# Kernel optimization log

Hardware: AMD Instinct MI355X
Metric: run time of the kernel (lower is better)

The kernel has to match this reference:

```python
import jax, jax.numpy as jnp
import numpy as np

D_MODEL = 1024
LN_EPS = 1e-5


def setup_inputs() -> dict:
    key = jax.random.key(0)
    ks = jax.random.split(key, 12)
    d = D_MODEL
    std_qkv = np.sqrt(2.0 / (d + d / 16)).astype(np.float32)
    std_fc = np.sqrt(2.0 / (d + d)).astype(np.float32)  # xavier_normal for square matrix
    inp = {
        "x": jax.random.normal(ks[0], (2, 2048, d), dtype=jnp.float32),
        "Wq": jax.random.normal(ks[1], (d, d), dtype=jnp.float32) * std_qkv,
        "bq": jnp.zeros((d,), dtype=jnp.float32),
        "Wk": jax.random.normal(ks[2], (d, d), dtype=jnp.float32) * std_qkv,
        "bk": jnp.zeros((d,), dtype=jnp.float32),
        "Wv": jax.random.normal(ks[3], (d, d), dtype=jnp.float32) * std_qkv,
        "bv": jnp.zeros((d,), dtype=jnp.float32),
        "Wfc": jax.random.normal(ks[4], (d, d), dtype=jnp.float32) * std_fc,
        "bfc": jnp.zeros((d,), dtype=jnp.float32),
        "gamma": jnp.ones((d,), dtype=jnp.float32),
        "beta": jnp.zeros((d,), dtype=jnp.float32),
        "n_heads": 16,
    }
    return inp


def reference(x, Wq, bq, Wk, bk, Wv, bv, Wfc, bfc, gamma, beta, n_heads):
    b, l, d = x.shape
    dk = d // n_heads

    def proj2(t, W, bias):
        # Faithful to original: projection applied TWICE (w_qs(w_qs(input)) etc.)
        t = t @ W.T + bias
        return t @ W.T + bias

    def split_heads(t):
        # b l (h dk) -> h b l dk
        return t.reshape(b, l, n_heads, dk).transpose(2, 0, 1, 3)

    q = split_heads(proj2(x, Wq, bq))
    k = split_heads(proj2(x, Wk, bk))
    v = split_heads(proj2(x, Wv, bv))

    scores = jnp.einsum("hblk,hbtk->hblt", q, k) / np.sqrt(dk).astype(np.float32)
    attn = jax.nn.softmax(scores, axis=3)
    out = jnp.einsum("hblt,hbtv->hblv", attn, v)
    out = out.transpose(1, 2, 0, 3).reshape(b, l, d)  # h b l v -> b l (h v)
    out = out @ Wfc.T + bfc  # dropout = identity in eval
    out = out + x

    mu = jnp.mean(out, axis=-1, keepdims=True)
    var = jnp.mean(jnp.square(out - mu), axis=-1, keepdims=True)
    out = (out - mu) * jax.lax.rsqrt(var + LN_EPS) * gamma + beta
    return (out, attn)
```

## Files before the change

kernel.cpp:

```cpp
#include <hip/hip_runtime.h>
#include <hip/hip_bf16.h>

typedef unsigned short u16;
typedef float  f32x4  __attribute__((ext_vector_type(4)));
typedef short  bf16x8 __attribute__((ext_vector_type(8)));
typedef u16    u16x4  __attribute__((ext_vector_type(4)));
typedef u16    u16x8  __attribute__((ext_vector_type(8)));

__device__ __forceinline__ u16 f2bf(float f) {
    union { __hip_bfloat16 b; u16 u; } c;
    c.b = __float2bfloat16(f);
    return c.u;
}
__device__ __forceinline__ float bf2f(u16 u) {
    union { unsigned i; float f; } c;
    c.i = ((unsigned)u) << 16;
    return c.f;
}

__device__ __forceinline__ void gl2lds16(const u16* g, u16* l) {
    __builtin_amdgcn_global_load_lds(
        (const __attribute__((address_space(1))) void*)g,
        (__attribute__((address_space(3))) void*)l,
        16, 0, 0);
}

__global__ __launch_bounds__(256) void convk(const float* __restrict__ src,
                                             u16* __restrict__ dst, int n4) {
    int i = blockIdx.x * 256 + threadIdx.x;
    if (i < n4) {
        float4 v = ((const float4*)src)[i];
        u16x4 o = { f2bf(v.x), f2bf(v.y), f2bf(v.z), f2bf(v.w) };
        ((u16x4*)dst)[i] = o;
    }
}

__global__ __launch_bounds__(256) void convW(const float* __restrict__ Wq,
                                             const float* __restrict__ Wk,
                                             const float* __restrict__ Wv,
                                             const float* __restrict__ Wfc,
                                             u16* __restrict__ Wallb,
                                             u16* __restrict__ Wfcb) {
    const int z = blockIdx.y;
    const float* src = z == 0 ? Wq : z == 1 ? Wk : z == 2 ? Wv : Wfc;
    u16* dst = z < 3 ? Wallb + (size_t)z * 1048576 : Wfcb;
    int i = blockIdx.x * 256 + threadIdx.x;
    float4 v = ((const float4*)src)[i];
    u16x4 o = { f2bf(v.x), f2bf(v.y), f2bf(v.z), f2bf(v.w) };
    ((u16x4*)dst)[i] = o;
}

__global__ __launch_bounds__(256) void transkB(const float* __restrict__ Wq,
                                               const float* __restrict__ Wk,
                                               const float* __restrict__ Wv,
                                               u16* __restrict__ Wallt) {
    const int z = blockIdx.z;
    const float* src = z == 0 ? Wq : z == 1 ? Wk : Wv;
    u16* dst = Wallt + (size_t)z * 1048576;
    __shared__ u16 t[64][72];
    const int tr = blockIdx.x * 64, tc = blockIdx.y * 64;
    const int r4 = threadIdx.x >> 4;
    const int c4 = (threadIdx.x & 15) * 4;
#pragma unroll
    for (int rr = 0; rr < 4; ++rr) {
        int r = rr * 16 + r4;
        float4 v = *(const float4*)&src[(size_t)(tr + r) * 1024 + tc + c4];
        t[r][c4] = f2bf(v.x); t[r][c4 + 1] = f2bf(v.y);
        t[r][c4 + 2] = f2bf(v.z); t[r][c4 + 3] = f2bf(v.w);
    }
    __syncthreads();
#pragma unroll
    for (int rr = 0; rr < 4; ++rr) {
        int oc = rr * 16 + r4;
        u16x4 o = { t[c4][oc], t[c4 + 1][oc], t[c4 + 2][oc], t[c4 + 3][oc] };
        *(u16x4*)&dst[(size_t)(tc + oc) * 1024 + tr + c4] = o;
    }
}

__global__ __launch_bounds__(256) void transV(const u16* __restrict__ QKV,
                                              u16* __restrict__ VT) {
    const int kt = blockIdx.x, bb = blockIdx.y, h = blockIdx.z;
    __shared__ u16 t[64][72];
    const int tid = threadIdx.x;
    {
        const int key = tid >> 3, d8 = (tid & 7) * 8;
        const u16* src = QKV + 2048 +
            ((size_t)(bb * 2048 + kt * 64 + key)) * 3072 + h * 64 + d8;
        *(u16x8*)&t[key][d8]      = *(const u16x8*)src;
        *(u16x8*)&t[key + 32][d8] = *(const u16x8*)(src + (size_t)32 * 3072);
    }
    __syncthreads();
    {
        const int dk = tid >> 3, k8 = (tid & 7) * 8;
        u16* dst = VT + ((size_t)((bb * 16 + h) * 64 + dk)) * 2048 + kt * 64 + k8;
        u16x8 o0, o1;
#pragma unroll
        for (int j = 0; j < 8; ++j) { o0[j] = t[k8 + j][dk]; o1[j] = t[k8 + j][dk + 32]; }
        *(u16x8*)dst = o0;
        *(u16x8*)(dst + (size_t)32 * 2048) = o1;
    }
}

__global__ __launch_bounds__(256) void bias2(const float* __restrict__ Wq, const float* __restrict__ bq,
                                             const float* __restrict__ Wk, const float* __restrict__ bk,
                                             const float* __restrict__ Wv, const float* __restrict__ bv,
                                             float* __restrict__ out) {
    const int z = blockIdx.y;
    const float* W = z == 0 ? Wq : z == 1 ? Wk : Wv;
    const float* b = z == 0 ? bq : z == 1 ? bk : bv;
    const int row  = blockIdx.x * 4 + (threadIdx.x >> 6);
    const int lane = threadIdx.x & 63;
    float4 w  = ((const float4*)(W + (size_t)row * 1024))[lane];
    float4 bb = ((const float4*)b)[lane];
    float s = w.x * bb.x + w.y * bb.y + w.z * bb.z + w.w * bb.w;
#pragma unroll
    for (int d = 1; d < 64; d <<= 1) s += __shfl_xor(s, d);
    if (lane == 0) out[z * 1024 + row] = s + b[row];
}

template<int OUTF32>
__global__ __launch_bounds__(256) void gemm_bt(const u16* __restrict__ A,
                                               const u16* __restrict__ B,
                                               const float* __restrict__ bias,
                                               void* __restrict__ Cout,
                                               int M, int N, int K,
                                               size_t zA, size_t zB, size_t zC) {
    __shared__ __align__(16) u16 As[128 * 32];
    __shared__ __align__(16) u16 Bs[128 * 32];

    const int tid  = threadIdx.x;
    const int lane = tid & 63;
    const int w    = tid >> 6;
    const int lr   = lane & 15;
    const int lg   = lane >> 4;
    const int wr   = (w >> 1) * 64;
    const int wc   = (w & 1) * 64;
    const int bm   = blockIdx.x * 128;
    const int bn   = blockIdx.y * 128;
    const int z    = blockIdx.z;
    A += (size_t)z * zA;
    B += (size_t)z * zB;
    char* Cz = (char*)Cout + (size_t)z * zC * (OUTF32 ? 4 : 2);

    const int srow = w * 32 + (lane >> 2);
    const int scol = (lane & 3) * 8;
    u16* la = &As[(w * 32) * 32];
    u16* lb = &Bs[(w * 32) * 32];

    f32x4 acc[4][4] = {};

    for (int k0 = 0; k0 < K; k0 += 32) {
        const u16* Ag = A + (size_t)(bm + srow) * K + k0 + scol;
        const u16* Bg = B + (size_t)(bn + srow) * K + k0 + scol;
        gl2lds16(Ag, la);
        gl2lds16(Ag + (size_t)16 * K, la + 16 * 32);
        gl2lds16(Bg, lb);
        gl2lds16(Bg + (size_t)16 * K, lb + 16 * 32);
        __syncthreads();

        bf16x8 af[4], bfr[4];
#pragma unroll
        for (int i = 0; i < 4; ++i)
            af[i] = *(const bf16x8*)&As[(wr + i * 16 + lr) * 32 + lg * 8];
#pragma unroll
        for (int j = 0; j < 4; ++j)
            bfr[j] = *(const bf16x8*)&Bs[(wc + j * 16 + lr) * 32 + lg * 8];
#pragma unroll
        for (int i = 0; i < 4; ++i)
#pragma unroll
            for (int j = 0; j < 4; ++j)
                acc[i][j] = __builtin_amdgcn_mfma_f32_16x16x32_bf16(
                    af[i], bfr[j], acc[i][j], 0, 0, 0);
        __syncthreads();
    }

#pragma unroll
    for (int i = 0; i < 4; ++i) {
        const int grow = bm + wr + i * 16 + lg * 4;
#pragma unroll
        for (int j = 0; j < 4; ++j) {
            const int gcol = bn + wc + j * 16 + lr;
            const float bv = bias ? bias[gcol] : 0.f;
#pragma unroll
            for (int r = 0; r < 4; ++r) {
                float v = acc[i][j][r] + bv;
                if (OUTF32)
                    ((float*)Cz)[(size_t)(grow + r) * N + gcol] = v;
                else
                    ((u16*)Cz)[(size_t)(grow + r) * N + gcol] = f2bf(v);
            }
        }
    }
}

__global__ __launch_bounds__(256, 4) void attn3(const u16* __restrict__ QKV,
                                                const u16* __restrict__ VT,
                                                float* __restrict__ P,
                                                u16* __restrict__ O) {
    const int hw  = blockIdx.x;
    const int L   = (hw & 7) * 128 + (hw >> 3);
    const int qb  = L & 31;
    const int bbh = L >> 5;
    const int bb  = bbh >> 4;
    const int h   = bbh & 15;
    const int tid = threadIdx.x, lane = tid & 63, w = tid >> 6;
    const int lr = lane & 15, lg = lane >> 4;

    __shared__ __align__(16) u16 Ks[2][64 * 64];
    __shared__ __align__(16) u16 Vs[2][64 * 64];
    __shared__ __align__(16) u16 Ps[4][16 * 64];

    const int qrow0 = qb * 64 + w * 16;
    const size_t qoff = ((size_t)bb * 2048 + qrow0 + lr) * 3072 + h * 64 + lg * 8;
    const bf16x8 qf0 = *(const bf16x8*)&QKV[qoff];
    const bf16x8 qf1 = *(const bf16x8*)&QKV[qoff + 32];

    const int srow  = lane >> 3;
    const int sslot = (lane & 7) ^ srow;
    const u16* kg0 = QKV + 1024 + ((size_t)bb * 2048 + w * 16 + srow) * 3072 + h * 64 + sslot * 8;
    const u16* vg0 = VT + ((size_t)((bb * 16 + h) * 64) + w * 16 + srow) * 2048 + sslot * 8;

    const int swz   = (lr & 7) << 3;
    const int offk0 = (lg * 8) ^ swz;
    const int offk1 = (32 + lg * 8) ^ swz;
    const int rowB  = lr * 64;
    const float SC  = 0.18033688011112042f;

    auto stageK = [&](int kt, int buf) {
        const u16* s = kg0 + (size_t)kt * 64 * 3072;
        gl2lds16(s,                   &Ks[buf][(w * 16) * 64]);
        gl2lds16(s + (size_t)8 * 3072, &Ks[buf][(w * 16 + 8) * 64]);
    };
    auto stageV = [&](int kt, int buf) {
        const u16* s = vg0 + kt * 64;
        gl2lds16(s,                   &Vs[buf][(w * 16) * 64]);
        gl2lds16(s + (size_t)8 * 2048, &Vs[buf][(w * 16 + 8) * 64]);
    };

    float lsum[4] = {0.f, 0.f, 0.f, 0.f};
    stageK(0, 0);
    for (int kt = 0; kt < 32; ++kt) {
        const int cur = kt & 1;
        if (kt < 31) {
            stageK(kt + 1, cur ^ 1);
            asm volatile("s_waitcnt vmcnt(2)" ::: "memory");
        } else {
            asm volatile("s_waitcnt vmcnt(0)" ::: "memory");
        }
        __builtin_amdgcn_s_barrier();
#pragma unroll
        for (int jb = 0; jb < 4; ++jb) {
            bf16x8 kf0 = *(const bf16x8*)&Ks[cur][jb * 1024 + rowB + offk0];
            bf16x8 kf1 = *(const bf16x8*)&Ks[cur][jb * 1024 + rowB + offk1];
            f32x4 acc = {0.f, 0.f, 0.f, 0.f};
            acc = __builtin_amdgcn_mfma_f32_16x16x32_bf16(qf0, kf0, acc, 0, 0, 0);
            acc = __builtin_amdgcn_mfma_f32_16x16x32_bf16(qf1, kf1, acc, 0, 0, 0);
#pragma unroll
            for (int r = 0; r < 4; ++r)
                lsum[r] += __builtin_amdgcn_exp2f(acc[r] * SC);
        }
        __builtin_amdgcn_s_barrier();
    }
#pragma unroll
    for (int r = 0; r < 4; ++r) {
#pragma unroll
        for (int d = 1; d < 16; d <<= 1) lsum[r] += __shfl_xor(lsum[r], d);
    }
    float rl[4];
#pragma unroll
    for (int r = 0; r < 4; ++r) rl[r] = 1.f / lsum[r];

    f32x4 oacc[4] = {};
    const size_t prowb = (size_t)(h * 2 + bb) * 2048 + qrow0;
    const int wrr = lane >> 2;
    const int wc0 = (lane & 3) * 4;

    stageK(0, 0); stageV(0, 0);
    for (int kt = 0; kt < 32; ++kt) {
        const int cur = kt & 1;
        if (kt == 0) {
            stageK(1, 1); stageV(1, 1);
            asm volatile("s_waitcnt vmcnt(4)" ::: "memory");
        } else if (kt < 31) {
            stageK(kt + 1, cur ^ 1); stageV(kt + 1, cur ^ 1);
            asm volatile("s_waitcnt vmcnt(8)" ::: "memory");
        } else {
            asm volatile("s_waitcnt vmcnt(4)" ::: "memory");
        }
        __builtin_amdgcn_s_barrier();

#pragma unroll
        for (int jb = 0; jb < 4; ++jb) {
            bf16x8 kf0 = *(const bf16x8*)&Ks[cur][jb * 1024 + rowB + offk0];
            bf16x8 kf1 = *(const bf16x8*)&Ks[cur][jb * 1024 + rowB + offk1];
            f32x4 acc = {0.f, 0.f, 0.f, 0.f};
            acc = __builtin_amdgcn_mfma_f32_16x16x32_bf16(qf0, kf0, acc, 0, 0, 0);
            acc = __builtin_amdgcn_mfma_f32_16x16x32_bf16(qf1, kf1, acc, 0, 0, 0);
#pragma unroll
            for (int r = 0; r < 4; ++r) {
                float p = __builtin_amdgcn_exp2f(acc[r] * SC) * rl[r];
                const int row = lg * 4 + r;
                Ps[w][row * 64 + ((jb * 16 + lr) ^ ((row & 7) << 3))] = f2bf(p);
            }
        }
#pragma unroll
        for (int kk = 0; kk < 2; ++kk) {
            const int offk = kk ? offk1 : offk0;
            bf16x8 pa = *(const bf16x8*)&Ps[w][rowB + offk];
#pragma unroll
            for (int dkb = 0; dkb < 4; ++dkb) {
                bf16x8 vb = *(const bf16x8*)&Vs[cur][dkb * 1024 + rowB + offk];
                oacc[dkb] = __builtin_amdgcn_mfma_f32_16x16x32_bf16(pa, vb, oacc[dkb], 0, 0, 0);
            }
        }
#pragma unroll
        for (int k4 = 0; k4 < 4; ++k4) {
            const int c = wc0 + 16 * k4;
            const int s = c >> 3, e = c & 7;
            u16x4 pb = *(const u16x4*)&Ps[w][wrr * 64 + ((s ^ (wrr & 7)) * 8) + e];
            f32x4 pv = { bf2f(pb[0]), bf2f(pb[1]), bf2f(pb[2]), bf2f(pb[3]) };
            __builtin_nontemporal_store(pv,
                (f32x4*)&P[(prowb + wrr) * 2048 + kt * 64 + c]);
        }
        __builtin_amdgcn_s_barrier();
    }

#pragma unroll
    for (int dkb = 0; dkb < 4; ++dkb)
#pragma unroll
        for (int r = 0; r < 4; ++r)
            O[((size_t)bb * 2048 + qrow0 + lg * 4 + r) * 1024 + h * 64 + dkb * 16 + lr] =
                f2bf(oacc[dkb][r]);
}

__global__ __launch_bounds__(256) void resid_ln(float* __restrict__ Y,
                                                const float* __restrict__ x,
                                                const float* __restrict__ gamma,
                                                const float* __restrict__ beta) {
    const int row = blockIdx.x, tid = threadIdx.x;
    const int lane = tid & 63, w = tid >> 6;
    float4 y  = ((const float4*)(Y + (size_t)row * 1024))[tid];
    float4 xv = ((const float4*)(x + (size_t)row * 1024))[tid];
    float t0 = y.x + xv.x, t1 = y.y + xv.y, t2 = y.z + xv.z, t3 = y.w + xv.w;
    float s  = t0 + t1 + t2 + t3;
    float ss = t0 * t0 + t1 * t1 + t2 * t2 + t3 * t3;
#pragma unroll
    for (int d = 1; d < 64; d <<= 1) { s += __shfl_xor(s, d); ss += __shfl_xor(ss, d); }
    __shared__ float as_[4], aq_[4];
    if (lane == 0) { as_[w] = s; aq_[w] = ss; }
    __syncthreads();
    s  = as_[0] + as_[1] + as_[2] + as_[3];
    ss = aq_[0] + aq_[1] + aq_[2] + aq_[3];
    const float mu  = s * (1.f / 1024.f);
    const float var = ss * (1.f / 1024.f) - mu * mu;
    const float rs  = rsqrtf(var + 1e-5f);
    float4 g  = ((const float4*)gamma)[tid];
    float4 be = ((const float4*)beta)[tid];
    float4 o;
    o.x = (t0 - mu) * rs * g.x + be.x;
    o.y = (t1 - mu) * rs * g.y + be.y;
    o.z = (t2 - mu) * rs * g.z + be.z;
    o.w = (t3 - mu) * rs * g.w + be.w;
    ((float4*)(Y + (size_t)row * 1024))[tid] = o;
}

extern "C" void kernel_launch(void* const* d_in, const int* in_sizes, int n_in,
                              void* d_out, int out_size, void* d_ws, size_t ws_size,
                              hipStream_t stream) {
    const float* x     = (const float*)d_in[0];
    const float* Wq    = (const float*)d_in[1];
    const float* bq    = (const float*)d_in[2];
    const float* Wk    = (const float*)d_in[3];
    const float* bk    = (const float*)d_in[4];
    const float* Wv    = (const float*)d_in[5];
    const float* bv    = (const float*)d_in[6];
    const float* Wfc   = (const float*)d_in[7];
    const float* bfc   = (const float*)d_in[8];
    const float* gamma = (const float*)d_in[9];
    const float* beta  = (const float*)d_in[10];

    float* out  = (float*)d_out;
    float* attn = out + (size_t)4194304;

    u16* VT = (u16*)d_out;

    char* ws = (char*)d_ws;
    u16* QKV  = (u16*)(ws);
    u16* Ob   = (u16*)(ws + (size_t)24 * 1048576);
    u16* Wfcb = (u16*)(ws + (size_t)32 * 1048576);

    char* sc = (char*)attn;
    u16*   Xb    = (u16*)sc;
    u16*   Wallb = (u16*)(sc + (size_t)8  * 1048576);
    u16*   Wallt = (u16*)(sc + (size_t)14 * 1048576);
    u16*   Wall2 = (u16*)(sc + (size_t)20 * 1048576);
    float* ball2 = (float*)(sc + (size_t)26 * 1048576);

    const size_t WSZ = 1048576;

    convk<<<4096, 256, 0, stream>>>(x, Xb, 1048576);
    convW<<<dim3(1024, 4), 256, 0, stream>>>(Wq, Wk, Wv, Wfc, Wallb, Wfcb);
    transkB<<<dim3(16, 16, 3), 256, 0, stream>>>(Wq, Wk, Wv, Wallt);
    bias2<<<dim3(256, 3), 256, 0, stream>>>(Wq, bq, Wk, bk, Wv, bv, ball2);

    const dim3 blk(256);
    gemm_bt<0><<<dim3(8, 8, 3), blk, 0, stream>>>(Wallb, Wallt, nullptr, Wall2,
                                                  1024, 1024, 1024, WSZ, WSZ, WSZ);
    gemm_bt<0><<<dim3(32, 24), blk, 0, stream>>>(Xb, Wall2, ball2, QKV,
                                                 4096, 3072, 1024, 0, 0, 0);

    transV<<<dim3(32, 2, 16), 256, 0, stream>>>(QKV, VT);
    attn3<<<1024, 256, 0, stream>>>(QKV, VT, attn, Ob);

    gemm_bt<1><<<dim3(32, 8), blk, 0, stream>>>(Ob, Wfcb, bfc, out,
                                                4096, 1024, 1024, 0, 0, 0);
    resid_ln<<<4096, 256, 0, stream>>>(out, x, gamma, beta);
}
```

Before: 326.7 us.

## Double per-wave query rows in attention and fuse residual add into FC GEMM

The attention kernel now has each wave process 32 query rows instead of 16, so a block covers 128 rows and the grid halves. Each K/V tile staged in LDS is therefore reused across twice as many queries, which cuts global K/V traffic, at the cost of more registers (occupancy hint lowered from 4 to 3) and a larger P staging buffer. Separately, the residual add of x moves into the FC GEMM epilogue, so the layernorm kernel no longer reads x.

```diff
diff --git a/kernel.cpp b/kernel.cpp
--- a/kernel.cpp
+++ b/kernel.cpp
@@ -124,7 +124,8 @@
                                                const float* __restrict__ bias,
                                                void* __restrict__ Cout,
                                                int M, int N, int K,
-                                               size_t zA, size_t zB, size_t zC) {
+                                               size_t zA, size_t zB, size_t zC,
+                                               const float* __restrict__ xres) {
     __shared__ __align__(16) u16 As[128 * 32];
     __shared__ __align__(16) u16 Bs[128 * 32];
 
@@ -184,23 +185,25 @@
 #pragma unroll
             for (int r = 0; r < 4; ++r) {
                 float v = acc[i][j][r] + bv;
-                if (OUTF32)
+                if (OUTF32) {
+                    if (xres) v += xres[(size_t)(grow + r) * N + gcol];
                     ((float*)Cz)[(size_t)(grow + r) * N + gcol] = v;
-                else
+                } else {
                     ((u16*)Cz)[(size_t)(grow + r) * N + gcol] = f2bf(v);
+                }
             }
         }
     }
 }
 
-__global__ __launch_bounds__(256, 4) void attn3(const u16* __restrict__ QKV,
+__global__ __launch_bounds__(256, 3) void attn4(const u16* __restrict__ QKV,
                                                 const u16* __restrict__ VT,
                                                 float* __restrict__ P,
                                                 u16* __restrict__ O) {
     const int hw  = blockIdx.x;
-    const int L   = (hw & 7) * 128 + (hw >> 3);
-    const int qb  = L & 31;
-    const int bbh = L >> 5;
+    const int L   = (hw & 7) * 64 + (hw >> 3);
+    const int qb  = L & 15;
+    const int bbh = L >> 4;
     const int bb  = bbh >> 4;
     const int h   = bbh & 15;
     const int tid = threadIdx.x, lane = tid & 63, w = tid >> 6;
@@ -208,12 +211,17 @@
 
     __shared__ __align__(16) u16 Ks[2][64 * 64];
     __shared__ __align__(16) u16 Vs[2][64 * 64];
-    __shared__ __align__(16) u16 Ps[4][16 * 64];
-
-    const int qrow0 = qb * 64 + w * 16;
-    const size_t qoff = ((size_t)bb * 2048 + qrow0 + lr) * 3072 + h * 64 + lg * 8;
-    const bf16x8 qf0 = *(const bf16x8*)&QKV[qoff];
-    const bf16x8 qf1 = *(const bf16x8*)&QKV[qoff + 32];
+    __shared__ __align__(16) u16 Ps[4][32 * 64];
+
+    const int qrow0 = qb * 128 + w * 32;
+    bf16x8 qf[2][2];
+#pragma unroll
+    for (int qg = 0; qg < 2; ++qg) {
+        const size_t qoff =
+            ((size_t)bb * 2048 + qrow0 + qg * 16 + lr) * 3072 + h * 64 + lg * 8;
+        qf[qg][0] = *(const bf16x8*)&QKV[qoff];
+        qf[qg][1] = *(const bf16x8*)&QKV[qoff + 32];
+    }
 
     const int srow  = lane >> 3;
     const int sslot = (lane & 7) ^ srow;
@@ -228,16 +236,16 @@
 
     auto stageK = [&](int kt, int buf) {
         const u16* s = kg0 + (size_t)kt * 64 * 3072;
-        gl2lds16(s,                   &Ks[buf][(w * 16) * 64]);
+        gl2lds16(s,                    &Ks[buf][(w * 16) * 64]);
         gl2lds16(s + (size_t)8 * 3072, &Ks[buf][(w * 16 + 8) * 64]);
     };
     auto stageV = [&](int kt, int buf) {
         const u16* s = vg0 + kt * 64;
-        gl2lds16(s,                   &Vs[buf][(w * 16) * 64]);
+        gl2lds16(s,                    &Vs[buf][(w * 16) * 64]);
         gl2lds16(s + (size_t)8 * 2048, &Vs[buf][(w * 16 + 8) * 64]);
     };
 
-    float lsum[4] = {0.f, 0.f, 0.f, 0.f};
+    float lsum[2][4] = {};
     stageK(0, 0);
     for (int kt = 0; kt < 32; ++kt) {
         const int cur = kt & 1;
@@ -252,25 +260,33 @@
         for (int jb = 0; jb < 4; ++jb) {
             bf16x8 kf0 = *(const bf16x8*)&Ks[cur][jb * 1024 + rowB + offk0];
             bf16x8 kf1 = *(const bf16x8*)&Ks[cur][jb * 1024 + rowB + offk1];
-            f32x4 acc = {0.f, 0.f, 0.f, 0.f};
-            acc = __builtin_amdgcn_mfma_f32_16x16x32_bf16(qf0, kf0, acc, 0, 0, 0);
-            acc = __builtin_amdgcn_mfma_f32_16x16x32_bf16(qf1, kf1, acc, 0, 0, 0);
-#pragma unroll
-            for (int r = 0; r < 4; ++r)
-                lsum[r] += __builtin_amdgcn_exp2f(acc[r] * SC);
+#pragma unroll
+            for (int qg = 0; qg < 2; ++qg) {
+                f32x4 acc = {0.f, 0.f, 0.f, 0.f};
+                acc = __builtin_amdgcn_mfma_f32_16x16x32_bf16(qf[qg][0], kf0, acc, 0, 0, 0);
+                acc = __builtin_amdgcn_mfma_f32_16x16x32_bf16(qf[qg][1], kf1, acc, 0, 0, 0);
+#pragma unroll
+                for (int r = 0; r < 4; ++r)
+                    lsum[qg][r] += __builtin_amdgcn_exp2f(acc[r] * SC);
+            }
         }
         __builtin_amdgcn_s_barrier();
     }
 #pragma unroll
-    for (int r = 0; r < 4; ++r) {
-#pragma unroll
-        for (int d = 1; d < 16; d <<= 1) lsum[r] += __shfl_xor(lsum[r], d);
-    }
-    float rl[4];
-#pragma unroll
-    for (int r = 0; r < 4; ++r) rl[r] = 1.f / lsum[r];
-
-    f32x4 oacc[4] = {};
+    for (int qg = 0; qg < 2; ++qg)
+#pragma unroll
+        for (int r = 0; r < 4; ++r) {
+#pragma unroll
+            for (int d = 1; d < 16; d <<= 1)
+                lsum[qg][r] += __shfl_xor(lsum[qg][r], d);
+        }
+    float rl[2][4];
+#pragma unroll
+    for (int qg = 0; qg < 2; ++qg)
+#pragma unroll
+        for (int r = 0; r < 4; ++r) rl[qg][r] = 1.f / lsum[qg][r];
+
+    f32x4 oacc[2][4] = {};
     const size_t prowb = (size_t)(h * 2 + bb) * 2048 + qrow0;
     const int wrr = lane >> 2;
     const int wc0 = (lane & 3) * 4;
@@ -283,9 +299,9 @@
             asm volatile("s_waitcnt vmcnt(4)" ::: "memory");
         } else if (kt < 31) {
             stageK(kt + 1, cur ^ 1); stageV(kt + 1, cur ^ 1);
+            asm volatile("s_waitcnt vmcnt(12)" ::: "memory");
+        } else {
             asm volatile("s_waitcnt vmcnt(8)" ::: "memory");
-        } else {
-            asm volatile("s_waitcnt vmcnt(4)" ::: "memory");
         }
         __builtin_amdgcn_s_barrier();
 
@@ -293,55 +309,65 @@
         for (int jb = 0; jb < 4; ++jb) {
             bf16x8 kf0 = *(const bf16x8*)&Ks[cur][jb * 1024 + rowB + offk0];
             bf16x8 kf1 = *(const bf16x8*)&Ks[cur][jb * 1024 + rowB + offk1];
-            f32x4 acc = {0.f, 0.f, 0.f, 0.f};
-            acc = __builtin_amdgcn_mfma_f32_16x16x32_bf16(qf0, kf0, acc, 0, 0, 0);
-            acc = __builtin_amdgcn_mfma_f32_16x16x32_bf16(qf1, kf1, acc, 0, 0, 0);
-#pragma unroll
-            for (int r = 0; r < 4; ++r) {
-                float p = __builtin_amdgcn_exp2f(acc[r] * SC) * rl[r];
-                const int row = lg * 4 + r;
-                Ps[w][row * 64 + ((jb * 16 + lr) ^ ((row & 7) << 3))] = f2bf(p);
+#pragma unroll
+            for (int qg = 0; qg < 2; ++qg) {
+                f32x4 acc = {0.f, 0.f, 0.f, 0.f};
+                acc = __builtin_amdgcn_mfma_f32_16x16x32_bf16(qf[qg][0], kf0, acc, 0, 0, 0);
+                acc = __builtin_amdgcn_mfma_f32_16x16x32_bf16(qf[qg][1], kf1, acc, 0, 0, 0);
+#pragma unroll
+                for (int r = 0; r < 4; ++r) {
+                    float p = __builtin_amdgcn_exp2f(acc[r] * SC) * rl[qg][r];
+                    const int row = qg * 16 + lg * 4 + r;
+                    Ps[w][row * 64 + ((jb * 16 + lr) ^ ((row & 7) << 3))] = f2bf(p);
+                }
             }
         }
 #pragma unroll
-        for (int kk = 0; kk < 2; ++kk) {
-            const int offk = kk ? offk1 : offk0;
-            bf16x8 pa = *(const bf16x8*)&Ps[w][rowB + offk];
-#pragma unroll
-            for (int dkb = 0; dkb < 4; ++dkb) {
-                bf16x8 vb = *(const bf16x8*)&Vs[cur][dkb * 1024 + rowB + offk];
-                oacc[dkb] = __builtin_amdgcn_mfma_f32_16x16x32_bf16(pa, vb, oacc[dkb], 0, 0, 0);
+        for (int qg = 0; qg < 2; ++qg)
+#pragma unroll
+            for (int kk = 0; kk < 2; ++kk) {
+                const int offk = kk ? offk1 : offk0;
+                bf16x8 pa = *(const bf16x8*)&Ps[w][(qg * 16 + lr) * 64 + offk];
+#pragma unroll
+                for (int dkb = 0; dkb < 4; ++dkb) {
+                    bf16x8 vb = *(const bf16x8*)&Vs[cur][dkb * 1024 + rowB + offk];
+                    oacc[qg][dkb] =
+                        __builtin_amdgcn_mfma_f32_16x16x32_bf16(pa, vb, oacc[qg][dkb], 0, 0, 0);
+                }
             }
-        }
-#pragma unroll
-        for (int k4 = 0; k4 < 4; ++k4) {
-            const int c = wc0 + 16 * k4;
-            const int s = c >> 3, e = c & 7;
-            u16x4 pb = *(const u16x4*)&Ps[w][wrr * 64 + ((s ^ (wrr & 7)) * 8) + e];
-            f32x4 pv = { bf2f(pb[0]), bf2f(pb[1]), bf2f(pb[2]), bf2f(pb[3]) };
-            __builtin_nontemporal_store(pv,
-                (f32x4*)&P[(prowb + wrr) * 2048 + kt * 64 + c]);
+#pragma unroll
+        for (int rg = 0; rg < 2; ++rg) {
+            const int wr2 = wrr + rg * 16;
+#pragma unroll
+            for (int k4 = 0; k4 < 4; ++k4) {
+                const int c = wc0 + 16 * k4;
+                const int s = c >> 3, e = c & 7;
+                u16x4 pb = *(const u16x4*)&Ps[w][wr2 * 64 + ((s ^ (wr2 & 7)) * 8) + e];
+                f32x4 pv = { bf2f(pb[0]), bf2f(pb[1]), bf2f(pb[2]), bf2f(pb[3]) };
+                __builtin_nontemporal_store(pv,
+                    (f32x4*)&P[(prowb + wr2) * 2048 + kt * 64 + c]);
+            }
         }
         __builtin_amdgcn_s_barrier();
     }
 
 #pragma unroll
-    for (int dkb = 0; dkb < 4; ++dkb)
-#pragma unroll
-        for (int r = 0; r < 4; ++r)
-            O[((size_t)bb * 2048 + qrow0 + lg * 4 + r) * 1024 + h * 64 + dkb * 16 + lr] =
-                f2bf(oacc[dkb][r]);
-}
-
-__global__ __launch_bounds__(256) void resid_ln(float* __restrict__ Y,
-                                                const float* __restrict__ x,
-                                                const float* __restrict__ gamma,
-                                                const float* __restrict__ beta) {
+    for (int qg = 0; qg < 2; ++qg)
+#pragma unroll
+        for (int dkb = 0; dkb < 4; ++dkb)
+#pragma unroll
+            for (int r = 0; r < 4; ++r)
+                O[((size_t)bb * 2048 + qrow0 + qg * 16 + lg * 4 + r) * 1024 +
+                  h * 64 + dkb * 16 + lr] = f2bf(oacc[qg][dkb][r]);
+}
+
+__global__ __launch_bounds__(256) void ln_only(float* __restrict__ Y,
+                                               const float* __restrict__ gamma,
+                                               const float* __restrict__ beta) {
     const int row = blockIdx.x, tid = threadIdx.x;
     const int lane = tid & 63, w = tid >> 6;
-    float4 y  = ((const float4*)(Y + (size_t)row * 1024))[tid];
-    float4 xv = ((const float4*)(x + (size_t)row * 1024))[tid];
-    float t0 = y.x + xv.x, t1 = y.y + xv.y, t2 = y.z + xv.z, t3 = y.w + xv.w;
+    float4 y = ((const float4*)(Y + (size_t)row * 1024))[tid];
+    float t0 = y.x, t1 = y.y, t2 = y.z, t3 = y.w;
     float s  = t0 + t1 + t2 + t3;
     float ss = t0 * t0 + t1 * t1 + t2 * t2 + t3 * t3;
 #pragma unroll
@@ -405,14 +431,14 @@
 
     const dim3 blk(256);
     gemm_bt<0><<<dim3(8, 8, 3), blk, 0, stream>>>(Wallb, Wallt, nullptr, Wall2,
-                                                  1024, 1024, 1024, WSZ, WSZ, WSZ);
+                                                  1024, 1024, 1024, WSZ, WSZ, WSZ, nullptr);
     gemm_bt<0><<<dim3(32, 24), blk, 0, stream>>>(Xb, Wall2, ball2, QKV,
-                                                 4096, 3072, 1024, 0, 0, 0);
+                                                 4096, 3072, 1024, 0, 0, 0, nullptr);
 
     transV<<<dim3(32, 2, 16), 256, 0, stream>>>(QKV, VT);
-    attn3<<<1024, 256, 0, stream>>>(QKV, VT, attn, Ob);
+    attn4<<<512, 256, 0, stream>>>(QKV, VT, attn, Ob);
 
     gemm_bt<1><<<dim3(32, 8), blk, 0, stream>>>(Ob, Wfcb, bfc, out,
-                                                4096, 1024, 1024, 0, 0, 0);
-    resid_ln<<<4096, 256, 0, stream>>>(out, x, gamma, beta);
-}
+                                                4096, 1024, 1024, 0, 0, 0, x);
+    ln_only<<<4096, 256, 0, stream>>>(out, gamma, beta);
+}
```

Measured after the change: 354.4 us. +8.5%, slower.

## Triple-buffer attention K pass, reorder P store, fuse residual into FC GEMM

Applied to the files above, without the earlier changes.

The first attention pass moves to a three-buffer K ring with prefetch distance two, which drops one barrier per iteration. The second pass now writes the P tile to global memory before the PV MFMAs, and s_setprio raises wave priority around the MFMA sections. Shared memory is merged into one array. The residual add moves into the FC GEMM epilogue, so the layernorm kernel no longer reads x. The aim is to cut barrier stalls, overlap the global P stores with compute, and save one pass over x, at the cost of an extra read inside the GEMM epilogue and more pipeline complexity.

```diff
diff --git a/kernel.cpp b/kernel.cpp
--- a/kernel.cpp
+++ b/kernel.cpp
@@ -124,7 +124,8 @@
                                                const float* __restrict__ bias,
                                                void* __restrict__ Cout,
                                                int M, int N, int K,
-                                               size_t zA, size_t zB, size_t zC) {
+                                               size_t zA, size_t zB, size_t zC,
+                                               const float* __restrict__ xres) {
     __shared__ __align__(16) u16 As[128 * 32];
     __shared__ __align__(16) u16 Bs[128 * 32];
 
@@ -184,16 +185,18 @@
 #pragma unroll
             for (int r = 0; r < 4; ++r) {
                 float v = acc[i][j][r] + bv;
-                if (OUTF32)
+                if (OUTF32) {
+                    if (xres) v += xres[(size_t)(grow + r) * N + gcol];
                     ((float*)Cz)[(size_t)(grow + r) * N + gcol] = v;
-                else
+                } else {
                     ((u16*)Cz)[(size_t)(grow + r) * N + gcol] = f2bf(v);
+                }
             }
         }
     }
 }
 
-__global__ __launch_bounds__(256, 4) void attn3(const u16* __restrict__ QKV,
+__global__ __launch_bounds__(256, 4) void attn5(const u16* __restrict__ QKV,
                                                 const u16* __restrict__ VT,
                                                 float* __restrict__ P,
                                                 u16* __restrict__ O) {
@@ -206,9 +209,7 @@
     const int tid = threadIdx.x, lane = tid & 63, w = tid >> 6;
     const int lr = lane & 15, lg = lane >> 4;
 
-    __shared__ __align__(16) u16 Ks[2][64 * 64];
-    __shared__ __align__(16) u16 Vs[2][64 * 64];
-    __shared__ __align__(16) u16 Ps[4][16 * 64];
+    __shared__ __align__(16) u16 smem[20480];
 
     const int qrow0 = qb * 64 + w * 16;
     const size_t qoff = ((size_t)bb * 2048 + qrow0 + lr) * 3072 + h * 64 + lg * 8;
@@ -226,32 +227,30 @@
     const int rowB  = lr * 64;
     const float SC  = 0.18033688011112042f;
 
-    auto stageK = [&](int kt, int buf) {
+    auto stageKto = [&](int kt, int ldsOff) {
         const u16* s = kg0 + (size_t)kt * 64 * 3072;
-        gl2lds16(s,                   &Ks[buf][(w * 16) * 64]);
-        gl2lds16(s + (size_t)8 * 3072, &Ks[buf][(w * 16 + 8) * 64]);
+        gl2lds16(s,                    smem + ldsOff + (w * 16) * 64);
+        gl2lds16(s + (size_t)8 * 3072, smem + ldsOff + (w * 16 + 8) * 64);
     };
-    auto stageV = [&](int kt, int buf) {
+    auto stageVto = [&](int kt, int ldsOff) {
         const u16* s = vg0 + kt * 64;
-        gl2lds16(s,                   &Vs[buf][(w * 16) * 64]);
-        gl2lds16(s + (size_t)8 * 2048, &Vs[buf][(w * 16 + 8) * 64]);
+        gl2lds16(s,                    smem + ldsOff + (w * 16) * 64);
+        gl2lds16(s + (size_t)8 * 2048, smem + ldsOff + (w * 16 + 8) * 64);
     };
 
     float lsum[4] = {0.f, 0.f, 0.f, 0.f};
-    stageK(0, 0);
+    stageKto(0, 0);
+    stageKto(1, 4096);
     for (int kt = 0; kt < 32; ++kt) {
-        const int cur = kt & 1;
-        if (kt < 31) {
-            stageK(kt + 1, cur ^ 1);
-            asm volatile("s_waitcnt vmcnt(2)" ::: "memory");
-        } else {
-            asm volatile("s_waitcnt vmcnt(0)" ::: "memory");
-        }
+        if (kt < 31) asm volatile("s_waitcnt vmcnt(2)" ::: "memory");
+        else         asm volatile("s_waitcnt vmcnt(0)" ::: "memory");
         __builtin_amdgcn_s_barrier();
+        const u16* Kb = smem + (kt % 3) * 4096;
+        __builtin_amdgcn_s_setprio(1);
 #pragma unroll
         for (int jb = 0; jb < 4; ++jb) {
-            bf16x8 kf0 = *(const bf16x8*)&Ks[cur][jb * 1024 + rowB + offk0];
-            bf16x8 kf1 = *(const bf16x8*)&Ks[cur][jb * 1024 + rowB + offk1];
+            bf16x8 kf0 = *(const bf16x8*)&Kb[jb * 1024 + rowB + offk0];
+            bf16x8 kf1 = *(const bf16x8*)&Kb[jb * 1024 + rowB + offk1];
             f32x4 acc = {0.f, 0.f, 0.f, 0.f};
             acc = __builtin_amdgcn_mfma_f32_16x16x32_bf16(qf0, kf0, acc, 0, 0, 0);
             acc = __builtin_amdgcn_mfma_f32_16x16x32_bf16(qf1, kf1, acc, 0, 0, 0);
@@ -259,7 +258,8 @@
             for (int r = 0; r < 4; ++r)
                 lsum[r] += __builtin_amdgcn_exp2f(acc[r] * SC);
         }
-        __builtin_amdgcn_s_barrier();
+        __builtin_amdgcn_s_setprio(0);
+        if (kt < 30) stageKto(kt + 2, ((kt + 2) % 3) * 4096);
     }
 #pragma unroll
     for (int r = 0; r < 4; ++r) {
@@ -269,30 +269,38 @@
     float rl[4];
 #pragma unroll
     for (int r = 0; r < 4; ++r) rl[r] = 1.f / lsum[r];
+
+    __syncthreads();
 
     f32x4 oacc[4] = {};
     const size_t prowb = (size_t)(h * 2 + bb) * 2048 + qrow0;
     const int wrr = lane >> 2;
     const int wc0 = (lane & 3) * 4;
-
-    stageK(0, 0); stageV(0, 0);
+    u16* Psw = smem + 16384 + w * 1024;
+
+    stageKto(0, 0); stageVto(0, 8192);
     for (int kt = 0; kt < 32; ++kt) {
         const int cur = kt & 1;
         if (kt == 0) {
-            stageK(1, 1); stageV(1, 1);
+            stageKto(1, 4096); stageVto(1, 12288);
             asm volatile("s_waitcnt vmcnt(4)" ::: "memory");
         } else if (kt < 31) {
-            stageK(kt + 1, cur ^ 1); stageV(kt + 1, cur ^ 1);
+            stageKto(kt + 1, (cur ^ 1) * 4096);
+            stageVto(kt + 1, 8192 + (cur ^ 1) * 4096);
             asm volatile("s_waitcnt vmcnt(8)" ::: "memory");
         } else {
             asm volatile("s_waitcnt vmcnt(4)" ::: "memory");
         }
         __builtin_amdgcn_s_barrier();
 
+        const u16* Kb = smem + cur * 4096;
+        const u16* Vb = smem + 8192 + cur * 4096;
+
+        __builtin_amdgcn_s_setprio(1);
 #pragma unroll
         for (int jb = 0; jb < 4; ++jb) {
-            bf16x8 kf0 = *(const bf16x8*)&Ks[cur][jb * 1024 + rowB + offk0];
-            bf16x8 kf1 = *(const bf16x8*)&Ks[cur][jb * 1024 + rowB + offk1];
+            bf16x8 kf0 = *(const bf16x8*)&Kb[jb * 1024 + rowB + offk0];
+            bf16x8 kf1 = *(const bf16x8*)&Kb[jb * 1024 + rowB + offk1];
             f32x4 acc = {0.f, 0.f, 0.f, 0.f};
             acc = __builtin_amdgcn_mfma_f32_16x16x32_bf16(qf0, kf0, acc, 0, 0, 0);
             acc = __builtin_amdgcn_mfma_f32_16x16x32_bf16(qf1, kf1, acc, 0, 0, 0);
@@ -300,28 +308,31 @@
             for (int r = 0; r < 4; ++r) {
                 float p = __builtin_amdgcn_exp2f(acc[r] * SC) * rl[r];
                 const int row = lg * 4 + r;
-                Ps[w][row * 64 + ((jb * 16 + lr) ^ ((row & 7) << 3))] = f2bf(p);
+                Psw[row * 64 + ((jb * 16 + lr) ^ ((row & 7) << 3))] = f2bf(p);
             }
         }
-#pragma unroll
-        for (int kk = 0; kk < 2; ++kk) {
-            const int offk = kk ? offk1 : offk0;
-            bf16x8 pa = *(const bf16x8*)&Ps[w][rowB + offk];
-#pragma unroll
-            for (int dkb = 0; dkb < 4; ++dkb) {
-                bf16x8 vb = *(const bf16x8*)&Vs[cur][dkb * 1024 + rowB + offk];
-                oacc[dkb] = __builtin_amdgcn_mfma_f32_16x16x32_bf16(pa, vb, oacc[dkb], 0, 0, 0);
-            }
-        }
+        __builtin_amdgcn_s_setprio(0);
 #pragma unroll
         for (int k4 = 0; k4 < 4; ++k4) {
             const int c = wc0 + 16 * k4;
             const int s = c >> 3, e = c & 7;
-            u16x4 pb = *(const u16x4*)&Ps[w][wrr * 64 + ((s ^ (wrr & 7)) * 8) + e];
+            u16x4 pb = *(const u16x4*)&Psw[wrr * 64 + ((s ^ (wrr & 7)) * 8) + e];
             f32x4 pv = { bf2f(pb[0]), bf2f(pb[1]), bf2f(pb[2]), bf2f(pb[3]) };
             __builtin_nontemporal_store(pv,
                 (f32x4*)&P[(prowb + wrr) * 2048 + kt * 64 + c]);
         }
+        __builtin_amdgcn_s_setprio(1);
+#pragma unroll
+        for (int kk = 0; kk < 2; ++kk) {
+            const int offk = kk ? offk1 : offk0;
+            bf16x8 pa = *(const bf16x8*)&Psw[rowB + offk];
+#pragma unroll
+            for (int dkb = 0; dkb < 4; ++dkb) {
+                bf16x8 vb = *(const bf16x8*)&Vb[dkb * 1024 + rowB + offk];
+                oacc[dkb] = __builtin_amdgcn_mfma_f32_16x16x32_bf16(pa, vb, oacc[dkb], 0, 0, 0);
+            }
+        }
+        __builtin_amdgcn_s_setprio(0);
         __builtin_amdgcn_s_barrier();
     }
 
@@ -333,15 +344,13 @@
                 f2bf(oacc[dkb][r]);
 }
 
-__global__ __launch_bounds__(256) void resid_ln(float* __restrict__ Y,
-                                                const float* __restrict__ x,
-                                                const float* __restrict__ gamma,
-                                                const float* __restrict__ beta) {
+__global__ __launch_bounds__(256) void ln_only(float* __restrict__ Y,
+                                               const float* __restrict__ gamma,
+                                               const float* __restrict__ beta) {
     const int row = blockIdx.x, tid = threadIdx.x;
     const int lane = tid & 63, w = tid >> 6;
-    float4 y  = ((const float4*)(Y + (size_t)row * 1024))[tid];
-    float4 xv = ((const float4*)(x + (size_t)row * 1024))[tid];
-    float t0 = y.x + xv.x, t1 = y.y + xv.y, t2 = y.z + xv.z, t3 = y.w + xv.w;
+    float4 y = ((const float4*)(Y + (size_t)row * 1024))[tid];
+    float t0 = y.x, t1 = y.y, t2 = y.z, t3 = y.w;
     float s  = t0 + t1 + t2 + t3;
     float ss = t0 * t0 + t1 * t1 + t2 * t2 + t3 * t3;
 #pragma unroll
@@ -405,14 +414,14 @@
 
     const dim3 blk(256);
     gemm_bt<0><<<dim3(8, 8, 3), blk, 0, stream>>>(Wallb, Wallt, nullptr, Wall2,
-                                                  1024, 1024, 1024, WSZ, WSZ, WSZ);
+                                                  1024, 1024, 1024, WSZ, WSZ, WSZ, nullptr);
     gemm_bt<0><<<dim3(32, 24), blk, 0, stream>>>(Xb, Wall2, ball2, QKV,
-                                                 4096, 3072, 1024, 0, 0, 0);
+                                                 4096, 3072, 1024, 0, 0, 0, nullptr);
 
     transV<<<dim3(32, 2, 16), 256, 0, stream>>>(QKV, VT);
-    attn3<<<1024, 256, 0, stream>>>(QKV, VT, attn, Ob);
+    attn5<<<1024, 256, 0, stream>>>(QKV, VT, attn, Ob);
 
     gemm_bt<1><<<dim3(32, 8), blk, 0, stream>>>(Ob, Wfcb, bfc, out,
-                                                4096, 1024, 1024, 0, 0, 0);
-    resid_ln<<<4096, 256, 0, stream>>>(out, x, gamma, beta);
-}
+                                                4096, 1024, 1024, 0, 0, 0, x);
+    ln_only<<<4096, 256, 0, stream>>>(out, gamma, beta);
+}
```

Measured after the change: 337.4 us. 1.03x slower.
